# Optimization experiments

Measured on AMD Instinct MI355X. Metric: run time of the kernel, lower is better.

## Reference

```python
import jax, jax.numpy as jnp
import numpy as np

NUM_HEADS = 16
THRESHOLD = 4e-4  # < 1/S so every softmax row keeps >=1 entry (classical path of grover_search_filter)


def setup_inputs() -> dict:
    key = jax.random.key(0)
    k0, k1, k2 = jax.random.split(key, 3)
    B, S, E = 4, 1024, 1024
    x = jax.random.normal(k0, (B, S, E), dtype=jnp.float32)
    Wqkv = jax.random.normal(k1, (3 * E, E), dtype=jnp.float32) * 0.02
    bqkv = jnp.zeros((3 * E,), dtype=jnp.float32)
    Wproj = jax.random.normal(k2, (E, E), dtype=jnp.float32) * 0.02
    bproj = jnp.zeros((E,), dtype=jnp.float32)
    return {"x": x, "Wqkv": Wqkv, "bqkv": bqkv, "Wproj": Wproj, "bproj": bproj}


def reference(x, Wqkv, bqkv, Wproj, bproj):
    B, S, E = x.shape
    H = NUM_HEADS
    D = E // H
    scale = D ** -0.5
    # qkv projection -> (3, B, H, S, D), matching torch permute(2,0,3,1,4)
    qkv = (x @ Wqkv.T + bqkv).reshape(B, S, 3, H, D).transpose(2, 0, 3, 1, 4)
    q, k, v = qkv[0], qkv[1], qkv[2]
    attn_logits = jnp.einsum("bhqd,bhkd->bhqk", q, k) * scale  # [B,H,S,S]
    attn_probs = jax.nn.softmax(attn_logits, axis=-1)
    # grover_search_filter: seq_len > 2**max_qubits -> classical threshold mask
    selected = attn_probs > THRESHOLD
    filtered_logits = jnp.where(selected, attn_logits, -jnp.inf)
    filtered_attn = jax.nn.softmax(filtered_logits, axis=-1)
    # dropout is identity in eval mode
    out = jnp.einsum("bhqk,bhkd->bhqd", filtered_attn, v)
    out = out.transpose(0, 2, 1, 3).reshape(B, S, E)
    out = out @ Wproj.T + bproj
    return out, filtered_attn
```

## Files before the change

kernel.cpp:

```cpp
#include <hip/hip_runtime.h>
#include <hip/hip_bf16.h>
#include <cstdint>


#define BB 4
#define SS 1024
#define EE 1024
#define HH 16
#define DD 64

typedef __attribute__((ext_vector_type(8))) short bf16x8;
typedef __attribute__((ext_vector_type(4))) float f32x4;

__global__ __launch_bounds__(256) void split_f32(
    const float* __restrict__ in, __hip_bfloat16* __restrict__ hi,
    __hip_bfloat16* __restrict__ lo, int n4) {
  int i = blockIdx.x * 256 + threadIdx.x;
  if (i >= n4) return;
  float4 v = ((const float4*)in)[i];
  float vv[4] = {v.x, v.y, v.z, v.w};
  __hip_bfloat16 h[4], l[4];
#pragma unroll
  for (int j = 0; j < 4; ++j) {
    h[j] = __float2bfloat16(vv[j]);
    l[j] = __float2bfloat16(vv[j] - __bfloat162float(h[j]));
  }
  ((ushort4*)hi)[i] = *(ushort4*)h;
  if (lo) ((ushort4*)lo)[i] = *(ushort4*)l;
}

template <int MODE>
__global__ __launch_bounds__(256) void gemm(
    const __hip_bfloat16* __restrict__ Ah, const __hip_bfloat16* __restrict__ Al,
    const __hip_bfloat16* __restrict__ Bh, const __hip_bfloat16* __restrict__ Bl,
    const float* __restrict__ Af, const float* __restrict__ bias,
    float* __restrict__ oF, __hip_bfloat16* __restrict__ o1,
    __hip_bfloat16* __restrict__ o2, __hip_bfloat16* __restrict__ o3,
    __hip_bfloat16* __restrict__ o4, __hip_bfloat16* __restrict__ o5,
    int M, int N, int K, int lda, int ldb, long long sA, long long sB) {
  constexpr bool SPLIT = (MODE == 0 || MODE == 1);
  constexpr bool AF32  = (MODE == 2);

  const int tid  = threadIdx.x;
  const int lane = tid & 63;
  const int wave = tid >> 6;
  const int wm   = (wave >> 1) * 64;
  const int wn   = (wave & 1) * 64;
  const int quad = lane >> 4;
  const int l15  = lane & 15;
  const int m0   = blockIdx.y * 128;
  const int n0   = blockIdx.x * 128;
  const long long zz = blockIdx.z;

  if (AF32) Af += zz * sA;
  else { Ah += zz * sA; if (SPLIT) Al += zz * sA; }
  Bh += zz * sB;
  if (SPLIT) Bl += zz * sB;

  __shared__ __align__(16) __hip_bfloat16 lds[(SPLIT ? 4 : 2) * 128 * 72];
  __hip_bfloat16* lAh = lds;
  __hip_bfloat16* lAl = SPLIT ? lds + 128 * 72 : nullptr;
  __hip_bfloat16* lBh = lds + (SPLIT ? 2 : 1) * 128 * 72;
  __hip_bfloat16* lBl = SPLIT ? lds + 3 * 128 * 72 : nullptr;

  f32x4 acc[4][4] = {};

  for (int k0 = 0; k0 < K; k0 += 64) {
#pragma unroll
    for (int it = 0; it < 4; ++it) {
      int flat = (it * 256 + tid) * 8;
      int row  = flat >> 6;
      int kk   = flat & 63;
      const bool mok = (m0 + row < M);
      const bool nok = (n0 + row < N);
      if (AF32) {
        float4 f0 = {0, 0, 0, 0}, f1 = {0, 0, 0, 0};
        if (mok) {
          const float* src = Af + (long long)(m0 + row) * lda + k0 + kk;
          f0 = *(const float4*)src;
          f1 = *(const float4*)(src + 4);
        }
        __hip_bfloat16 t[8];
        t[0] = __float2bfloat16(f0.x); t[1] = __float2bfloat16(f0.y);
        t[2] = __float2bfloat16(f0.z); t[3] = __float2bfloat16(f0.w);
        t[4] = __float2bfloat16(f1.x); t[5] = __float2bfloat16(f1.y);
        t[6] = __float2bfloat16(f1.z); t[7] = __float2bfloat16(f1.w);
        *(uint4*)&lAh[row * 72 + kk] = *(uint4*)t;
      } else {
        uint4 va = {0, 0, 0, 0};
        if (mok) va = *(const uint4*)(Ah + (long long)(m0 + row) * lda + k0 + kk);
        *(uint4*)&lAh[row * 72 + kk] = va;
        if (SPLIT) {
          uint4 vl = {0, 0, 0, 0};
          if (mok) vl = *(const uint4*)(Al + (long long)(m0 + row) * lda + k0 + kk);
          *(uint4*)&lAl[row * 72 + kk] = vl;
        }
      }
      uint4 vb = {0, 0, 0, 0};
      if (nok) vb = *(const uint4*)(Bh + (long long)(n0 + row) * ldb + k0 + kk);
      *(uint4*)&lBh[row * 72 + kk] = vb;
      if (SPLIT) {
        uint4 vbl = {0, 0, 0, 0};
        if (nok) vbl = *(const uint4*)(Bl + (long long)(n0 + row) * ldb + k0 + kk);
        *(uint4*)&lBl[row * 72 + kk] = vbl;
      }
    }
    __syncthreads();

#pragma unroll
    for (int ks = 0; ks < 64; ks += 32) {
      bf16x8 ah[4], bh[4], al[4], bl[4];
#pragma unroll
      for (int i = 0; i < 4; ++i) {
        int off = (wm + i * 16 + l15) * 72 + ks + quad * 8;
        ah[i] = *(const bf16x8*)&lAh[off];
        if (SPLIT) al[i] = *(const bf16x8*)&lAl[off];
      }
#pragma unroll
      for (int j = 0; j < 4; ++j) {
        int off = (wn + j * 16 + l15) * 72 + ks + quad * 8;
        bh[j] = *(const bf16x8*)&lBh[off];
        if (SPLIT) bl[j] = *(const bf16x8*)&lBl[off];
      }
#pragma unroll
      for (int i = 0; i < 4; ++i)
#pragma unroll
        for (int j = 0; j < 4; ++j) {
          if (SPLIT) {
            acc[i][j] = __builtin_amdgcn_mfma_f32_16x16x32_bf16(al[i], bh[j], acc[i][j], 0, 0, 0);
            acc[i][j] = __builtin_amdgcn_mfma_f32_16x16x32_bf16(ah[i], bl[j], acc[i][j], 0, 0, 0);
          }
          acc[i][j] = __builtin_amdgcn_mfma_f32_16x16x32_bf16(ah[i], bh[j], acc[i][j], 0, 0, 0);
        }
    }
    __syncthreads();
  }

#pragma unroll
  for (int i = 0; i < 4; ++i) {
#pragma unroll
    for (int j = 0; j < 4; ++j) {
#pragma unroll
      for (int r = 0; r < 4; ++r) {
        int m = m0 + wm + i * 16 + quad * 4 + r;
        int n = n0 + wn + j * 16 + l15;
        float v = acc[i][j][r];
        if (MODE == 0) {
          v += bias[n];
          int c = n >> 10, nn = n & 1023, h = nn >> 6, d = nn & 63;
          int b = m >> 10, s = m & 1023;
          long long idx = (((long long)(b * HH + h) * SS + s) << 6) + d;
          if (c == 0) {
            __hip_bfloat16 hh = __float2bfloat16(v);
            o1[idx] = hh;
            o2[idx] = __float2bfloat16(v - __bfloat162float(hh));
          } else if (c == 1) {
            __hip_bfloat16 hh = __float2bfloat16(v);
            o3[idx] = hh;
            o4[idx] = __float2bfloat16(v - __bfloat162float(hh));
          } else {
            o5[(((long long)(b * HH + h) * DD + d) << 10) + s] = __float2bfloat16(v);
          }
        } else if (MODE == 1) {
          oF[zz * (SS * SS) + (long long)m * SS + n] = v * 0.125f;
        } else if (MODE == 2) {
          if (n < DD) {
            int b = (int)(zz >> 4), h = (int)(zz & 15);
            o1[(((long long)(b * SS + m)) << 10) + h * DD + n] = __float2bfloat16(v);
          }
        } else {
          oF[(long long)m * EE + n] = v + bias[n];
        }
      }
    }
  }
}

__device__ __forceinline__ float wave_max64(float v) {
#pragma unroll
  for (int o = 32; o > 0; o >>= 1) v = fmaxf(v, __shfl_xor(v, o));
  return v;
}
__device__ __forceinline__ float wave_sum64(float v) {
#pragma unroll
  for (int o = 32; o > 0; o >>= 1) v += __shfl_xor(v, o);
  return v;
}

__global__ __launch_bounds__(256) void fused_attn(
    const __hip_bfloat16* __restrict__ qh, const __hip_bfloat16* __restrict__ ql,
    const __hip_bfloat16* __restrict__ kh, const __hip_bfloat16* __restrict__ kl,
    const __hip_bfloat16* __restrict__ vT, float* __restrict__ attn,
    __hip_bfloat16* __restrict__ ao) {
  const int tid  = threadIdx.x;
  const int lane = tid & 63;
  const int wave = tid >> 6;
  const int quad = lane >> 4;
  const int l15  = lane & 15;
  const int bh   = blockIdx.y;
  const int q0   = blockIdx.x * 16;
  const int brow = (bh >> 4) * SS;
  const int h    = bh & 15;
  const long long qbase = ((long long)bh * SS + q0) * DD;
  const long long kbase = (long long)bh * SS * DD;
  const long long vbase = (long long)bh * DD * SS;
  const long long abase = ((long long)bh * SS + q0) * SS;

  __shared__ __align__(16) float lg[16][1032];

  bf16x8 aqh[2], aql[2];
  {
    const __hip_bfloat16* ph = qh + qbase + l15 * DD + quad * 8;
    const __hip_bfloat16* pl = ql + qbase + l15 * DD + quad * 8;
    aqh[0] = *(const bf16x8*)(ph);
    aqh[1] = *(const bf16x8*)(ph + 32);
    aql[0] = *(const bf16x8*)(pl);
    aql[1] = *(const bf16x8*)(pl + 32);
  }

#pragma unroll
  for (int nt = 0; nt < 16; ++nt) {
    const int n = wave * 256 + nt * 16;
    const __hip_bfloat16* pkh = kh + kbase + (long long)(n + l15) * DD + quad * 8;
    const __hip_bfloat16* pkl = kl + kbase + (long long)(n + l15) * DD + quad * 8;
    bf16x8 bh0 = *(const bf16x8*)(pkh);
    bf16x8 bh1 = *(const bf16x8*)(pkh + 32);
    bf16x8 bl0 = *(const bf16x8*)(pkl);
    bf16x8 bl1 = *(const bf16x8*)(pkl + 32);
    f32x4 acc = {};
    acc = __builtin_amdgcn_mfma_f32_16x16x32_bf16(aql[0], bh0, acc, 0, 0, 0);
    acc = __builtin_amdgcn_mfma_f32_16x16x32_bf16(aqh[0], bl0, acc, 0, 0, 0);
    acc = __builtin_amdgcn_mfma_f32_16x16x32_bf16(aqh[0], bh0, acc, 0, 0, 0);
    acc = __builtin_amdgcn_mfma_f32_16x16x32_bf16(aql[1], bh1, acc, 0, 0, 0);
    acc = __builtin_amdgcn_mfma_f32_16x16x32_bf16(aqh[1], bl1, acc, 0, 0, 0);
    acc = __builtin_amdgcn_mfma_f32_16x16x32_bf16(aqh[1], bh1, acc, 0, 0, 0);
#pragma unroll
    for (int r = 0; r < 4; ++r) lg[quad * 4 + r][n + l15] = acc[r] * 0.125f;
  }
  __syncthreads();

#pragma unroll
  for (int rr = 0; rr < 4; ++rr) {
    const int row = wave * 4 + rr;
    float v[16];
#pragma unroll
    for (int i = 0; i < 16; ++i) v[i] = lg[row][lane + i * 64];
    float mloc = v[0];
#pragma unroll
    for (int t = 1; t < 16; ++t) mloc = fmaxf(mloc, v[t]);
    const float m = wave_max64(mloc);
    float e[16], zloc = 0.f;
#pragma unroll
    for (int t = 0; t < 16; ++t) { e[t] = expf(v[t] - m); zloc += e[t]; }
    const float Z = wave_sum64(zloc);
    float zsloc = 0.f;
    bool sel[16];
#pragma unroll
    for (int t = 0; t < 16; ++t) {
      sel[t] = (e[t] / Z) > 4e-4f;
      if (sel[t]) zsloc += e[t];
    }
    const float Zs = wave_sum64(zsloc);
    float* arow = attn + abase + (long long)row * SS;
    __hip_bfloat16* prow = (__hip_bfloat16*)&lg[row][0];
#pragma unroll
    for (int i = 0; i < 16; ++i) {
      const float w = sel[i] ? e[i] / Zs : 0.f;
      arow[lane + i * 64] = w;
      prow[lane + i * 64] = __float2bfloat16(w);
    }
  }
  __syncthreads();

  const int d0 = wave * 16;
  f32x4 oacc = {};
  const __hip_bfloat16* pv = vT + vbase + (long long)(d0 + l15) * SS + quad * 8;
  const __hip_bfloat16* pp = (const __hip_bfloat16*)&lg[l15][0] + quad * 8;
#pragma unroll
  for (int ks = 0; ks < 32; ++ks) {
    bf16x8 ap = *(const bf16x8*)(pp + ks * 32);
    bf16x8 bv = *(const bf16x8*)(pv + ks * 32);
    oacc = __builtin_amdgcn_mfma_f32_16x16x32_bf16(ap, bv, oacc, 0, 0, 0);
  }
#pragma unroll
  for (int r = 0; r < 4; ++r) {
    const int q = q0 + quad * 4 + r;
    ao[((long long)(brow + q)) * EE + h * DD + d0 + l15] = __float2bfloat16(oacc[r]);
  }
}

extern "C" void kernel_launch(void* const* d_in, const int* in_sizes, int n_in,
                              void* d_out, int out_size, void* d_ws, size_t ws_size,
                              hipStream_t stream) {
  const float* x     = (const float*)d_in[0];
  const float* Wqkv  = (const float*)d_in[1];
  const float* bqkv  = (const float*)d_in[2];
  const float* Wproj = (const float*)d_in[3];
  const float* bproj = (const float*)d_in[4];

  float* out   = (float*)d_out;
  float* attnF = out + (size_t)BB * SS * EE;

  const size_t M1 = 1024 * 1024;
  __hip_bfloat16* w = (__hip_bfloat16*)d_ws;

  if (ws_size >= (size_t)80 * 1024 * 1024) {
    __hip_bfloat16 *xh = w, *xl = xh + 4 * M1;
    __hip_bfloat16 *Wqh = xl + 4 * M1, *Wql = Wqh + 3 * M1, *Wph = Wql + 3 * M1;
    __hip_bfloat16 *qh = Wph + M1, *ql = qh + 4 * M1, *kh = ql + 4 * M1, *kl = kh + 4 * M1;
    __hip_bfloat16 *vT = kl + 4 * M1, *ao = vT + 4 * M1;

    split_f32<<<4096, 256, 0, stream>>>(x, xh, xl, 1024 * 1024);
    split_f32<<<3072, 256, 0, stream>>>(Wqkv, Wqh, Wql, 768 * 1024);
    split_f32<<<1024, 256, 0, stream>>>(Wproj, Wph, nullptr, 256 * 1024);

    gemm<0><<<dim3(24, 32, 1), 256, 0, stream>>>(
        xh, xl, Wqh, Wql, nullptr, bqkv, nullptr, qh, ql, kh, kl, vT,
        4096, 3072, 1024, 1024, 1024, 0LL, 0LL);
    fused_attn<<<dim3(SS / 16, BB * HH), 256, 0, stream>>>(
        qh, ql, kh, kl, vT, attnF, ao);
    gemm<3><<<dim3(8, 32, 1), 256, 0, stream>>>(
        ao, nullptr, Wph, nullptr, nullptr, bproj, out, nullptr, nullptr, nullptr, nullptr, nullptr,
        4096, 1024, 1024, 1024, 1024, 0LL, 0LL);
    return;
  }

  __hip_bfloat16 *Wqh = w, *Wql = Wqh + 3 * M1, *Wph = Wql + 3 * M1;
  __hip_bfloat16 *xh = Wph + M1, *xl = xh + M1;
  __hip_bfloat16 *qh = xl + M1, *ql = qh + M1, *kh = ql + M1, *kl = kh + M1;
  __hip_bfloat16 *vT = kl + M1, *ao = vT + M1;

  split_f32<<<3072, 256, 0, stream>>>(Wqkv, Wqh, Wql, 768 * 1024);
  split_f32<<<1024, 256, 0, stream>>>(Wproj, Wph, nullptr, 256 * 1024);

  for (int b = 0; b < BB; ++b) {
    const float* xb   = x + (size_t)b * SS * EE;
    float* attnb      = attnF + (size_t)b * HH * SS * SS;
    float* outb       = out + (size_t)b * SS * EE;

    split_f32<<<1024, 256, 0, stream>>>(xb, xh, xl, 256 * 1024);
    gemm<0><<<dim3(24, 8, 1), 256, 0, stream>>>(
        xh, xl, Wqh, Wql, nullptr, bqkv, nullptr, qh, ql, kh, kl, vT,
        1024, 3072, 1024, 1024, 1024, 0LL, 0LL);
    fused_attn<<<dim3(SS / 16, HH), 256, 0, stream>>>(
        qh, ql, kh, kl, vT, attnb, ao);
    gemm<3><<<dim3(8, 8, 1), 256, 0, stream>>>(
        ao, nullptr, Wph, nullptr, nullptr, bproj, outb, nullptr, nullptr, nullptr, nullptr, nullptr,
        1024, 1024, 1024, 1024, 1024, 0LL, 0LL);
  }
}
```

Measured before the change: 702.7 us.

## Keep attention logits in registers, cut LDS to bf16 probabilities, swizzle blocks

The fused attention kernel now keeps the QK^T accumulators in registers and computes softmax statistics there. It uses 16-lane shuffles plus a small cross-wave LDS reduction instead of staging fp32 logits in shared memory. LDS shrinks to a bf16 probability tile, which with launch_bounds(256,4) is meant to allow more resident blocks. The grid is flattened with an XCD-style block remap so neighbouring heads spread across dies. The threshold test now compares exp values against 4e-4*Z instead of dividing, and PV uses two accumulators for ILP. The trade-offs are higher register pressure and attn stores that are now strided by row per lane instead of coalesced.

```diff
diff --git a/kernel.cpp b/kernel.cpp
--- a/kernel.cpp
+++ b/kernel.cpp
@@ -176,18 +176,18 @@
   }
 }
 
-__device__ __forceinline__ float wave_max64(float v) {
-#pragma unroll
-  for (int o = 32; o > 0; o >>= 1) v = fmaxf(v, __shfl_xor(v, o));
+__device__ __forceinline__ float qg_max16(float v) {
+#pragma unroll
+  for (int o = 8; o > 0; o >>= 1) v = fmaxf(v, __shfl_xor(v, o));
   return v;
 }
-__device__ __forceinline__ float wave_sum64(float v) {
-#pragma unroll
-  for (int o = 32; o > 0; o >>= 1) v += __shfl_xor(v, o);
+__device__ __forceinline__ float qg_sum16(float v) {
+#pragma unroll
+  for (int o = 8; o > 0; o >>= 1) v += __shfl_xor(v, o);
   return v;
 }
 
-__global__ __launch_bounds__(256) void fused_attn(
+__global__ __launch_bounds__(256, 4) void fused_attn(
     const __hip_bfloat16* __restrict__ qh, const __hip_bfloat16* __restrict__ ql,
     const __hip_bfloat16* __restrict__ kh, const __hip_bfloat16* __restrict__ kl,
     const __hip_bfloat16* __restrict__ vT, float* __restrict__ attn,
@@ -197,8 +197,13 @@
   const int wave = tid >> 6;
   const int quad = lane >> 4;
   const int l15  = lane & 15;
-  const int bh   = blockIdx.y;
-  const int q0   = blockIdx.x * 16;
+
+  int id = blockIdx.x;
+  const int q8 = gridDim.x >> 3;
+  id = (id & 7) * q8 + (id >> 3);
+  const int bh = id >> 6;
+  const int q0 = (id & 63) * 16;
+
   const int brow = (bh >> 4) * SS;
   const int h    = bh & 15;
   const long long qbase = ((long long)bh * SS + q0) * DD;
@@ -206,86 +211,143 @@
   const long long vbase = (long long)bh * DD * SS;
   const long long abase = ((long long)bh * SS + q0) * SS;
 
-  __shared__ __align__(16) float lg[16][1032];
-
-  bf16x8 aqh[2], aql[2];
+  __shared__ __align__(16) __hip_bfloat16 Pl[16][1032];
+  __shared__ float red[3][4][16];
+
+  bf16x8 aqh0, aqh1, aql0, aql1;
   {
     const __hip_bfloat16* ph = qh + qbase + l15 * DD + quad * 8;
     const __hip_bfloat16* pl = ql + qbase + l15 * DD + quad * 8;
-    aqh[0] = *(const bf16x8*)(ph);
-    aqh[1] = *(const bf16x8*)(ph + 32);
-    aql[0] = *(const bf16x8*)(pl);
-    aql[1] = *(const bf16x8*)(pl + 32);
-  }
-
+    aqh0 = *(const bf16x8*)(ph);
+    aqh1 = *(const bf16x8*)(ph + 32);
+    aql0 = *(const bf16x8*)(pl);
+    aql1 = *(const bf16x8*)(pl + 32);
+  }
+
+  f32x4 acc[16];
+  const __hip_bfloat16* pkh0 = kh + kbase + (long long)(wave * 256 + l15) * DD + quad * 8;
+  const __hip_bfloat16* pkl0 = kl + kbase + (long long)(wave * 256 + l15) * DD + quad * 8;
 #pragma unroll
   for (int nt = 0; nt < 16; ++nt) {
-    const int n = wave * 256 + nt * 16;
-    const __hip_bfloat16* pkh = kh + kbase + (long long)(n + l15) * DD + quad * 8;
-    const __hip_bfloat16* pkl = kl + kbase + (long long)(n + l15) * DD + quad * 8;
-    bf16x8 bh0 = *(const bf16x8*)(pkh);
-    bf16x8 bh1 = *(const bf16x8*)(pkh + 32);
-    bf16x8 bl0 = *(const bf16x8*)(pkl);
-    bf16x8 bl1 = *(const bf16x8*)(pkl + 32);
-    f32x4 acc = {};
-    acc = __builtin_amdgcn_mfma_f32_16x16x32_bf16(aql[0], bh0, acc, 0, 0, 0);
-    acc = __builtin_amdgcn_mfma_f32_16x16x32_bf16(aqh[0], bl0, acc, 0, 0, 0);
-    acc = __builtin_amdgcn_mfma_f32_16x16x32_bf16(aqh[0], bh0, acc, 0, 0, 0);
-    acc = __builtin_amdgcn_mfma_f32_16x16x32_bf16(aql[1], bh1, acc, 0, 0, 0);
-    acc = __builtin_amdgcn_mfma_f32_16x16x32_bf16(aqh[1], bl1, acc, 0, 0, 0);
-    acc = __builtin_amdgcn_mfma_f32_16x16x32_bf16(aqh[1], bh1, acc, 0, 0, 0);
-#pragma unroll
-    for (int r = 0; r < 4; ++r) lg[quad * 4 + r][n + l15] = acc[r] * 0.125f;
+    const __hip_bfloat16* pkh = pkh0 + nt * 16 * DD;
+    const __hip_bfloat16* pkl = pkl0 + nt * 16 * DD;
+    bf16x8 b0 = *(const bf16x8*)(pkh);
+    bf16x8 b1 = *(const bf16x8*)(pkh + 32);
+    bf16x8 c0 = *(const bf16x8*)(pkl);
+    bf16x8 c1 = *(const bf16x8*)(pkl + 32);
+    f32x4 a = {};
+    a = __builtin_amdgcn_mfma_f32_16x16x32_bf16(aql0, b0, a, 0, 0, 0);
+    a = __builtin_amdgcn_mfma_f32_16x16x32_bf16(aqh0, c0, a, 0, 0, 0);
+    a = __builtin_amdgcn_mfma_f32_16x16x32_bf16(aqh0, b0, a, 0, 0, 0);
+    a = __builtin_amdgcn_mfma_f32_16x16x32_bf16(aql1, b1, a, 0, 0, 0);
+    a = __builtin_amdgcn_mfma_f32_16x16x32_bf16(aqh1, c1, a, 0, 0, 0);
+    a = __builtin_amdgcn_mfma_f32_16x16x32_bf16(aqh1, b1, a, 0, 0, 0);
+    acc[nt] = a;
+  }
+
+#pragma unroll
+  for (int nt = 0; nt < 16; ++nt)
+#pragma unroll
+    for (int r = 0; r < 4; ++r) acc[nt][r] *= 0.125f;
+
+  float mx[4];
+#pragma unroll
+  for (int r = 0; r < 4; ++r) {
+    float mm = acc[0][r];
+#pragma unroll
+    for (int nt = 1; nt < 16; ++nt) mm = fmaxf(mm, acc[nt][r]);
+    mx[r] = qg_max16(mm);
+  }
+  if (l15 == 0) {
+#pragma unroll
+    for (int r = 0; r < 4; ++r) red[0][wave][quad * 4 + r] = mx[r];
   }
   __syncthreads();
-
-#pragma unroll
-  for (int rr = 0; rr < 4; ++rr) {
-    const int row = wave * 4 + rr;
-    float v[16];
-#pragma unroll
-    for (int i = 0; i < 16; ++i) v[i] = lg[row][lane + i * 64];
-    float mloc = v[0];
-#pragma unroll
-    for (int t = 1; t < 16; ++t) mloc = fmaxf(mloc, v[t]);
-    const float m = wave_max64(mloc);
-    float e[16], zloc = 0.f;
-#pragma unroll
-    for (int t = 0; t < 16; ++t) { e[t] = expf(v[t] - m); zloc += e[t]; }
-    const float Z = wave_sum64(zloc);
-    float zsloc = 0.f;
-    bool sel[16];
-#pragma unroll
-    for (int t = 0; t < 16; ++t) {
-      sel[t] = (e[t] / Z) > 4e-4f;
-      if (sel[t]) zsloc += e[t];
+  float m[4];
+#pragma unroll
+  for (int r = 0; r < 4; ++r) {
+    const int q = quad * 4 + r;
+    m[r] = fmaxf(fmaxf(red[0][0][q], red[0][1][q]),
+                 fmaxf(red[0][2][q], red[0][3][q]));
+  }
+
+  float zl[4] = {0.f, 0.f, 0.f, 0.f};
+#pragma unroll
+  for (int nt = 0; nt < 16; ++nt)
+#pragma unroll
+    for (int r = 0; r < 4; ++r) {
+      float e = expf(acc[nt][r] - m[r]);
+      acc[nt][r] = e;
+      zl[r] += e;
     }
-    const float Zs = wave_sum64(zsloc);
-    float* arow = attn + abase + (long long)row * SS;
-    __hip_bfloat16* prow = (__hip_bfloat16*)&lg[row][0];
-#pragma unroll
-    for (int i = 0; i < 16; ++i) {
-      const float w = sel[i] ? e[i] / Zs : 0.f;
-      arow[lane + i * 64] = w;
-      prow[lane + i * 64] = __float2bfloat16(w);
+#pragma unroll
+  for (int r = 0; r < 4; ++r) zl[r] = qg_sum16(zl[r]);
+  if (l15 == 0) {
+#pragma unroll
+    for (int r = 0; r < 4; ++r) red[1][wave][quad * 4 + r] = zl[r];
+  }
+  __syncthreads();
+  float c[4];
+#pragma unroll
+  for (int r = 0; r < 4; ++r) {
+    const int q = quad * 4 + r;
+    const float Z = (red[1][0][q] + red[1][1][q]) + (red[1][2][q] + red[1][3][q]);
+    c[r] = 4e-4f * Z;
+  }
+
+  float sl[4] = {0.f, 0.f, 0.f, 0.f};
+#pragma unroll
+  for (int nt = 0; nt < 16; ++nt)
+#pragma unroll
+    for (int r = 0; r < 4; ++r)
+      if (acc[nt][r] > c[r]) sl[r] += acc[nt][r];
+#pragma unroll
+  for (int r = 0; r < 4; ++r) sl[r] = qg_sum16(sl[r]);
+  if (l15 == 0) {
+#pragma unroll
+    for (int r = 0; r < 4; ++r) red[2][wave][quad * 4 + r] = sl[r];
+  }
+  __syncthreads();
+  float rinv[4];
+#pragma unroll
+  for (int r = 0; r < 4; ++r) {
+    const int q = quad * 4 + r;
+    const float Zs = (red[2][0][q] + red[2][1][q]) + (red[2][2][q] + red[2][3][q]);
+    rinv[r] = 1.0f / Zs;
+  }
+
+#pragma unroll
+  for (int nt = 0; nt < 16; ++nt) {
+    const int k = wave * 256 + nt * 16 + l15;
+#pragma unroll
+    for (int r = 0; r < 4; ++r) {
+      const int q = quad * 4 + r;
+      const float e = acc[nt][r];
+      const float p = (e > c[r]) ? e * rinv[r] : 0.f;
+      attn[abase + (long long)q * SS + k] = p;
+      Pl[q][k] = __float2bfloat16(p);
     }
   }
   __syncthreads();
 
   const int d0 = wave * 16;
-  f32x4 oacc = {};
+  f32x4 o0 = {}, o1 = {};
   const __hip_bfloat16* pv = vT + vbase + (long long)(d0 + l15) * SS + quad * 8;
-  const __hip_bfloat16* pp = (const __hip_bfloat16*)&lg[l15][0] + quad * 8;
-#pragma unroll
-  for (int ks = 0; ks < 32; ++ks) {
-    bf16x8 ap = *(const bf16x8*)(pp + ks * 32);
-    bf16x8 bv = *(const bf16x8*)(pv + ks * 32);
-    oacc = __builtin_amdgcn_mfma_f32_16x16x32_bf16(ap, bv, oacc, 0, 0, 0);
+  const __hip_bfloat16* pp = &Pl[l15][0] + quad * 8;
+#pragma unroll
+  for (int ks = 0; ks < 32; ks += 2) {
+    bf16x8 a0 = *(const bf16x8*)(pp + ks * 32);
+    bf16x8 v0 = *(const bf16x8*)(pv + ks * 32);
+    o0 = __builtin_amdgcn_mfma_f32_16x16x32_bf16(a0, v0, o0, 0, 0, 0);
+    bf16x8 a1 = *(const bf16x8*)(pp + (ks + 1) * 32);
+    bf16x8 v1 = *(const bf16x8*)(pv + (ks + 1) * 32);
+    o1 = __builtin_amdgcn_mfma_f32_16x16x32_bf16(a1, v1, o1, 0, 0, 0);
   }
 #pragma unroll
   for (int r = 0; r < 4; ++r) {
     const int q = q0 + quad * 4 + r;
-    ao[((long long)(brow + q)) * EE + h * DD + d0 + l15] = __float2bfloat16(oacc[r]);
+    ao[((long long)(brow + q)) * EE + h * DD + d0 + l15] =
+        __float2bfloat16(o0[r] + o1[r]);
   }
 }
 
@@ -317,7 +379,7 @@
     gemm<0><<<dim3(24, 32, 1), 256, 0, stream>>>(
         xh, xl, Wqh, Wql, nullptr, bqkv, nullptr, qh, ql, kh, kl, vT,
         4096, 3072, 1024, 1024, 1024, 0LL, 0LL);
-    fused_attn<<<dim3(SS / 16, BB * HH), 256, 0, stream>>>(
+    fused_attn<<<dim3(BB * HH * 64), 256, 0, stream>>>(
         qh, ql, kh, kl, vT, attnF, ao);
     gemm<3><<<dim3(8, 32, 1), 256, 0, stream>>>(
         ao, nullptr, Wph, nullptr, nullptr, bproj, out, nullptr, nullptr, nullptr, nullptr, nullptr,
@@ -342,7 +404,7 @@
     gemm<0><<<dim3(24, 8, 1), 256, 0, stream>>>(
         xh, xl, Wqh, Wql, nullptr, bqkv, nullptr, qh, ql, kh, kl, vT,
         1024, 3072, 1024, 1024, 1024, 0LL, 0LL);
-    fused_attn<<<dim3(SS / 16, HH), 256, 0, stream>>>(
+    fused_attn<<<dim3(HH * 64), 256, 0, stream>>>(
         qh, ql, kh, kl, vT, attnb, ao);
     gemm<3><<<dim3(8, 8, 1), 256, 0, stream>>>(
         ao, nullptr, Wph, nullptr, nullptr, bproj, outb, nullptr, nullptr, nullptr, nullptr, nullptr,
```

Result: no change. 691.5 us (-1.6%).
